# Optimization experiments

Hardware: AMD Instinct MI355X
Metric: run time of the kernel (lower is better)

Reference implementation:

```python
import jax, jax.numpy as jnp
import numpy as np

N_EMBD = 1024
N_HEAD = 16
HEAD_DIM = N_EMBD // N_HEAD
B, T = 4, 1024
EPS = 1e-5


def _linear_params(key, fan_in, fan_out):
    kw, kb = jax.random.split(key)
    bound = 1.0 / np.sqrt(fan_in)
    W = jax.random.uniform(kw, (fan_in, fan_out), minval=-bound, maxval=bound, dtype=jnp.float32)
    b = jax.random.uniform(kb, (fan_out,), minval=-bound, maxval=bound, dtype=jnp.float32)
    return W, b


def setup_inputs() -> dict:
    key = jax.random.key(0)
    ks = jax.random.split(key, 8)
    x = jax.random.normal(ks[0], (B, T, N_EMBD), dtype=jnp.float32)
    Wq, bq = _linear_params(ks[1], N_EMBD, N_EMBD)
    Wk, bk = _linear_params(ks[2], N_EMBD, N_EMBD)
    Wv, bv = _linear_params(ks[3], N_EMBD, N_EMBD)
    Wp, bp = _linear_params(ks[4], N_EMBD, N_EMBD)
    W1, b1 = _linear_params(ks[5], N_EMBD, 4 * N_EMBD)
    W2, b2 = _linear_params(ks[6], 4 * N_EMBD, N_EMBD)
    g1 = jnp.ones((N_EMBD,), jnp.float32); be1 = jnp.zeros((N_EMBD,), jnp.float32)
    g2 = jnp.ones((N_EMBD,), jnp.float32); be2 = jnp.zeros((N_EMBD,), jnp.float32)
    return {"x": x, "Wq": Wq, "bq": bq, "Wk": Wk, "bk": bk, "Wv": Wv, "bv": bv,
            "Wp": Wp, "bp": bp, "W1": W1, "b1": b1, "W2": W2, "b2": b2,
            "g1": g1, "be1": be1, "g2": g2, "be2": be2}


def _layernorm(x, g, b):
    mu = jnp.mean(x, axis=-1, keepdims=True)
    var = jnp.mean(jnp.square(x - mu), axis=-1, keepdims=True)
    return (x - mu) * jax.lax.rsqrt(var + EPS) * g + b


def _attention(x, Wq, bq, Wk, bk, Wv, bv, Wp, bp):
    Bsz, Tt, C = x.shape
    def heads(W, b):
        return (x @ W + b).reshape(Bsz, Tt, N_HEAD, HEAD_DIM).transpose(0, 2, 1, 3)  # [B,H,T,d]
    q, k, v = heads(Wq, bq), heads(Wk, bk), heads(Wv, bv)
    scores = jnp.einsum('bhqd,bhkd->bhqk', q, k) / np.sqrt(HEAD_DIM).astype(np.float32)
    causal = jnp.tril(jnp.ones((Tt, Tt), dtype=bool))
    scores = jnp.where(causal, scores, -jnp.inf)
    attn = jax.nn.softmax(scores, axis=-1)
    out = jnp.einsum('bhqk,bhkd->bhqd', attn, v)  # [B,H,T,d]
    out = out.transpose(0, 2, 1, 3).reshape(Bsz, Tt, C)
    return out @ Wp + bp


def _ff(x, W1, b1, W2, b2):
    h = jax.nn.gelu(x @ W1 + b1, approximate=False)  # torch nn.GELU default = exact erf
    return h @ W2 + b2


def reference(x, Wq, bq, Wk, bk, Wv, bv, Wp, bp, W1, b1, W2, b2, g1, be1, g2, be2):
    x = x + _attention(_layernorm(x, g1, be1), Wq, bq, Wk, bk, Wv, bv, Wp, bp)
    x = x + _ff(_layernorm(x, g2, be2), W1, b1, W2, b2)
    return x
```

## Files before the change

### kernel.cpp

```cpp
#include <hip/hip_runtime.h>
#include <hip/hip_bf16.h>

typedef __attribute__((ext_vector_type(8))) __bf16 bf16x8;
typedef __attribute__((ext_vector_type(4))) float f32x4;
typedef __attribute__((ext_vector_type(4))) unsigned short u16x4;
typedef unsigned short u16;

#define AS3(p) ((__attribute__((address_space(3))) void*)(p))
#define AS1(p) ((const __attribute__((address_space(1))) void*)(p))

__device__ __forceinline__ u16 f2b(float f) {
    __hip_bfloat16 h = __float2bfloat16(f);
    return __builtin_bit_cast(u16, h);
}

__device__ __forceinline__ float gelu_exact(float v) {
    const float z = v * 0.70710678118654752f;
    const float a = fabsf(z);
    const float t = __builtin_amdgcn_rcpf(1.0f + 0.3275911f * a);
    float p = 1.061405429f;
    p = p * t - 1.453152027f;
    p = p * t + 1.421413741f;
    p = p * t - 0.284496736f;
    p = p * t + 0.254829592f;
    p = p * t;
    float erfv = 1.0f - p * __expf(-a * a);
    erfv = copysignf(erfv, z);
    return 0.5f * v * (1.0f + erfv);
}

__global__ __launch_bounds__(256) void transpose_w(
    const float* __restrict__ W, u16* __restrict__ WT, int K, int N)
{
    __shared__ u16 tile[32][33];
    const int tx = threadIdx.x & 31, ty = threadIdx.x >> 5;
    const int n0 = blockIdx.x * 32, k0 = blockIdx.y * 32;
    #pragma unroll
    for (int p = 0; p < 4; ++p)
        tile[ty + p * 8][tx] = f2b(W[(size_t)(k0 + ty + p * 8) * N + n0 + tx]);
    __syncthreads();
    #pragma unroll
    for (int p = 0; p < 4; ++p)
        WT[(size_t)(n0 + ty + p * 8) * K + k0 + tx] = tile[tx][ty + p * 8];
}

__global__ __launch_bounds__(256) void transpose_w3(
    const float* __restrict__ W0, const float* __restrict__ W1,
    const float* __restrict__ W2, u16* __restrict__ WT)
{
    __shared__ u16 tile[32][33];
    const int z = blockIdx.z;
    const float* W = (z == 0) ? W0 : (z == 1) ? W1 : W2;
    u16* dst = WT + (size_t)z * 1024 * 1024;
    const int tx = threadIdx.x & 31, ty = threadIdx.x >> 5;
    const int n0 = blockIdx.x * 32, k0 = blockIdx.y * 32;
    #pragma unroll
    for (int p = 0; p < 4; ++p)
        tile[ty + p * 8][tx] = f2b(W[(size_t)(k0 + ty + p * 8) * 1024 + n0 + tx]);
    __syncthreads();
    #pragma unroll
    for (int p = 0; p < 4; ++p)
        dst[(size_t)(n0 + ty + p * 8) * 1024 + k0 + tx] = tile[tx][ty + p * 8];
}

__global__ __launch_bounds__(256) void ln_bf16(
    const float* __restrict__ xin, const float* __restrict__ gam,
    const float* __restrict__ bet, u16* __restrict__ yout)
{
    __shared__ float red[8];
    const int row = blockIdx.x, tid = threadIdx.x;
    float4 v = ((const float4*)(xin + (size_t)row * 1024))[tid];
    float s = v.x + v.y + v.z + v.w;
    #pragma unroll
    for (int o = 32; o > 0; o >>= 1) s += __shfl_xor(s, o, 64);
    if ((tid & 63) == 0) red[tid >> 6] = s;
    __syncthreads();
    const float mu = (red[0] + red[1] + red[2] + red[3]) * (1.f / 1024.f);
    const float dx = v.x - mu, dy = v.y - mu, dz = v.z - mu, dw = v.w - mu;
    float sq = dx * dx + dy * dy + dz * dz + dw * dw;
    #pragma unroll
    for (int o = 32; o > 0; o >>= 1) sq += __shfl_xor(sq, o, 64);
    if ((tid & 63) == 0) red[4 + (tid >> 6)] = sq;
    __syncthreads();
    const float var = (red[4] + red[5] + red[6] + red[7]) * (1.f / 1024.f);
    const float inv = rsqrtf(var + 1e-5f);
    const float4 G = ((const float4*)gam)[tid];
    const float4 Bt = ((const float4*)bet)[tid];
    u16x4 o;
    o[0] = f2b(dx * inv * G.x + Bt.x);
    o[1] = f2b(dy * inv * G.y + Bt.y);
    o[2] = f2b(dz * inv * G.z + Bt.z);
    o[3] = f2b(dw * inv * G.w + Bt.w);
    ((u16x4*)(yout + (size_t)row * 1024))[tid] = o;
}

template <int MODE, int BM>
__global__ __launch_bounds__(256, (BM == 128 ? 3 : 2)) void gemm_bf16(
    const u16* __restrict__ A, const u16* __restrict__ BT,
    const float* __restrict__ b0, const float* __restrict__ b1,
    const float* __restrict__ b2, const float* __restrict__ resid,
    void* __restrict__ outp, int M, int N, int K)
{
    constexpr int WM = BM / 2;
    constexpr int MI = WM / 16;
    constexpr int NI = 4;
    constexpr int AJ = BM / 64;
    constexpr int AELEM = BM * 32;
    constexpr int BELEM = 128 * 32;
    __shared__ u16 Asm[3 * AELEM];
    __shared__ u16 Bsm[3 * BELEM];

    const int tid = threadIdx.x;
    const int lane = tid & 63, wid = tid >> 6;
    const int wm = wid >> 1, wn = wid & 1;
    const int g = lane >> 4, l16 = lane & 15;
    const int sx = (l16 >> 1) & 3;
    const int sslot = (lane & 3) ^ ((lane >> 3) & 3);

    const int nBN = N >> 7;
    const int cpx = gridDim.x >> 3;
    const int wg = (blockIdx.x & 7) * cpx + (blockIdx.x >> 3);
    const int bm0 = (wg / nBN) * BM, bn0 = (wg % nBN) * 128;

    f32x4 acc[MI][NI] = {};

    const u16* aBase = A + (size_t)(bm0 + (lane >> 2)) * K + sslot * 8;
    const u16* bBase = BT + (size_t)(bn0 + (lane >> 2)) * K + sslot * 8;

    auto stage = [&](int kt, int buf) {
        u16* adst = Asm + buf * AELEM + lane * 8;
        u16* bdst = Bsm + buf * BELEM + lane * 8;
        #pragma unroll
        for (int j = 0; j < AJ; ++j) {
            const int ia = wid * AJ + j;
            __builtin_amdgcn_global_load_lds(AS1(aBase + (size_t)(ia * 16) * K + kt),
                                             AS3(adst + ia * 512), 16, 0, 0);
        }
        #pragma unroll
        for (int j = 0; j < 2; ++j) {
            const int ib = wid * 2 + j;
            __builtin_amdgcn_global_load_lds(AS1(bBase + (size_t)(ib * 16) * K + kt),
                                             AS3(bdst + ib * 512), 16, 0, 0);
        }
    };

    const int nt = K / 32;
    stage(0, 0);
    stage(32, 1);
    int cur = 0, pre = 2;

    for (int t = 0; t < nt; ++t) {
        if (t + 1 < nt) {
            if constexpr (BM == 256) asm volatile("s_waitcnt vmcnt(6)" ::: "memory");
            else                     asm volatile("s_waitcnt vmcnt(4)" ::: "memory");
        } else {
            asm volatile("s_waitcnt vmcnt(0)" ::: "memory");
        }
        __builtin_amdgcn_s_barrier();
        __builtin_amdgcn_sched_barrier(0);

        const u16* asrc = Asm + cur * AELEM;
        const u16* bsrc = Bsm + cur * BELEM;
        bf16x8 af[MI], bfr[NI];
        #pragma unroll
        for (int mi = 0; mi < MI; ++mi) {
            const int r = wm * WM + mi * 16 + l16;
            af[mi] = *(const bf16x8*)(asrc + r * 32 + ((g ^ sx) << 3));
        }
        #pragma unroll
        for (int ni = 0; ni < NI; ++ni) {
            const int c = wn * 64 + ni * 16 + l16;
            bfr[ni] = *(const bf16x8*)(bsrc + c * 32 + ((g ^ sx) << 3));
        }
        if (t + 2 < nt) stage((t + 2) * 32, pre);

        #pragma unroll
        for (int mi = 0; mi < MI; ++mi)
            #pragma unroll
            for (int ni = 0; ni < NI; ++ni)
                acc[mi][ni] = __builtin_amdgcn_mfma_f32_16x16x32_bf16(
                    af[mi], bfr[ni], acc[mi][ni], 0, 0, 0);

        pre = cur;
        cur = (cur == 2) ? 0 : cur + 1;
    }

    #pragma unroll
    for (int mi = 0; mi < MI; ++mi) {
        #pragma unroll
        for (int ni = 0; ni < NI; ++ni) {
            #pragma unroll
            for (int j = 0; j < 4; ++j) {
                const int m = bm0 + wm * WM + mi * 16 + g * 4 + j;
                const int n = bn0 + wn * 64 + ni * 16 + l16;
                float v = acc[mi][ni][j];
                if constexpr (MODE == 0) {
                    const float bias = (n < 1024) ? b0[n]
                                      : (n < 2048) ? b1[n - 1024] : b2[n - 2048];
                    ((u16*)outp)[(size_t)m * N + n] = f2b(v + bias);
                } else if constexpr (MODE == 1) {
                    ((float*)outp)[(size_t)m * N + n] =
                        v + b0[n] + resid[(size_t)m * N + n];
                } else {
                    ((u16*)outp)[(size_t)m * N + n] = f2b(gelu_exact(v + b0[n]));
                }
            }
        }
    }
}

__global__ __launch_bounds__(256) void attn_fwd(
    const u16* __restrict__ qkv, u16* __restrict__ outp)
{
    __shared__ u16 Ksm[64 * 72];
    __shared__ u16 Vsm[64 * 72];
    __shared__ u16 Psm[4][16 * 72];
    const int tid = threadIdx.x, lane = tid & 63, w = tid >> 6;
    const int lin = blockIdx.y * 8 + blockIdx.x;
    const int xq = (lin >> 3) & 7;
    const int bh = (((lin >> 6) & 7) << 3) | (lin & 7);
    const int b = bh >> 4, h = bh & 15;
    const int g = lane >> 4, l16 = lane & 15;
    const int skv = tid >> 4;
    const int sd4 = (tid & 15) * 4;

    const u16* kvb = qkv + (size_t)(b * 1024) * 3072 + 1024 + h * 64;

    u16x4 kreg[4], vreg[4];
    auto issue = [&](int kv0) {
        const u16* kb = kvb + (size_t)kv0 * 3072;
        #pragma unroll
        for (int i = 0; i < 4; ++i)
            kreg[i] = *(const u16x4*)(kb + (size_t)(skv + 16 * i) * 3072 + sd4);
        #pragma unroll
        for (int i = 0; i < 4; ++i)
            vreg[i] = *(const u16x4*)(kb + (size_t)(4 * skv + i) * 3072 + 1024 + sd4);
    };

    #pragma unroll
    for (int half = 0; half < 2; ++half) {
        const int qt = half ? (15 - xq) : xq;
        const int q0 = qt * 64;

        bf16x8 qf0, qf1;
        {
            const u16* qp = qkv + (size_t)(b * 1024 + q0 + w * 16 + l16) * 3072
                            + h * 64 + g * 8;
            qf0 = *(const bf16x8*)qp;
            qf1 = *(const bf16x8*)(qp + 32);
        }
        float m_run[4] = {-1e30f, -1e30f, -1e30f, -1e30f};
        float l_run[4] = {0.f, 0.f, 0.f, 0.f};
        f32x4 oacc[4] = {};

        issue(0);

        for (int kvt = 0; kvt <= qt; ++kvt) {
            const int kv0 = kvt * 64;
            __syncthreads();
            #pragma unroll
            for (int i = 0; i < 4; ++i)
                *(u16x4*)(Ksm + (skv + 16 * i) * 72 + sd4) = kreg[i];
            #pragma unroll
            for (int j = 0; j < 4; ++j) {
                u16x4 t;
                t[0] = vreg[0][j]; t[1] = vreg[1][j];
                t[2] = vreg[2][j]; t[3] = vreg[3][j];
                *(u16x4*)(Vsm + (sd4 + j) * 72 + 4 * skv) = t;
            }
            __syncthreads();
            if (kvt < qt) issue(kv0 + 64);

            f32x4 s[4];
            #pragma unroll
            for (int t = 0; t < 4; ++t) {
                const bf16x8 kf0 = *(const bf16x8*)(Ksm + (t * 16 + l16) * 72 + g * 8);
                const bf16x8 kf1 = *(const bf16x8*)(Ksm + (t * 16 + l16) * 72 + 32 + g * 8);
                f32x4 z = {};
                z = __builtin_amdgcn_mfma_f32_16x16x32_bf16(qf0, kf0, z, 0, 0, 0);
                z = __builtin_amdgcn_mfma_f32_16x16x32_bf16(qf1, kf1, z, 0, 0, 0);
                s[t] = z;
            }
            float mx[4] = {-1e30f, -1e30f, -1e30f, -1e30f};
            #pragma unroll
            for (int t = 0; t < 4; ++t)
                #pragma unroll
                for (int j = 0; j < 4; ++j) {
                    const int qrow = q0 + w * 16 + g * 4 + j;
                    const int kvc = kv0 + t * 16 + l16;
                    float v = s[t][j] * 0.125f;
                    if (kvc > qrow) v = -1e30f;
                    s[t][j] = v;
                    mx[j] = fmaxf(mx[j], v);
                }
            #pragma unroll
            for (int o = 1; o < 16; o <<= 1)
                #pragma unroll
                for (int j = 0; j < 4; ++j)
                    mx[j] = fmaxf(mx[j], __shfl_xor(mx[j], o, 16));
            float alpha[4], rs[4];
            #pragma unroll
            for (int j = 0; j < 4; ++j) {
                const float mn = fmaxf(m_run[j], mx[j]);
                alpha[j] = __expf(m_run[j] - mn);
                m_run[j] = mn;
                rs[j] = 0.f;
            }
            #pragma unroll
            for (int t = 0; t < 4; ++t)
                #pragma unroll
                for (int j = 0; j < 4; ++j) {
                    const float p = __expf(s[t][j] - m_run[j]);
                    s[t][j] = p;
                    rs[j] += p;
                }
            #pragma unroll
            for (int o = 1; o < 16; o <<= 1)
                #pragma unroll
                for (int j = 0; j < 4; ++j)
                    rs[j] += __shfl_xor(rs[j], o, 16);
            #pragma unroll
            for (int j = 0; j < 4; ++j)
                l_run[j] = l_run[j] * alpha[j] + rs[j];
            #pragma unroll
            for (int dt = 0; dt < 4; ++dt)
                #pragma unroll
                for (int j = 0; j < 4; ++j)
                    oacc[dt][j] *= alpha[j];
            #pragma unroll
            for (int t = 0; t < 4; ++t)
                #pragma unroll
                for (int j = 0; j < 4; ++j)
                    Psm[w][(g * 4 + j) * 72 + t * 16 + l16] = f2b(s[t][j]);
            const bf16x8 pf0 = *(const bf16x8*)(&Psm[w][l16 * 72 + g * 8]);
            const bf16x8 pf1 = *(const bf16x8*)(&Psm[w][l16 * 72 + 32 + g * 8]);
            #pragma unroll
            for (int dt = 0; dt < 4; ++dt) {
                const bf16x8 vf0 = *(const bf16x8*)(Vsm + (dt * 16 + l16) * 72 + g * 8);
                const bf16x8 vf1 = *(const bf16x8*)(Vsm + (dt * 16 + l16) * 72 + 32 + g * 8);
                oacc[dt] = __builtin_amdgcn_mfma_f32_16x16x32_bf16(pf0, vf0, oacc[dt], 0, 0, 0);
                oacc[dt] = __builtin_amdgcn_mfma_f32_16x16x32_bf16(pf1, vf1, oacc[dt], 0, 0, 0);
            }
        }
        #pragma unroll
        for (int dt = 0; dt < 4; ++dt)
            #pragma unroll
            for (int j = 0; j < 4; ++j) {
                const int m = b * 1024 + q0 + w * 16 + g * 4 + j;
                const int col = h * 64 + dt * 16 + l16;
                outp[(size_t)m * 1024 + col] = f2b(oacc[dt][j] / l_run[j]);
            }
    }
}

extern "C" void kernel_launch(void* const* d_in, const int* in_sizes, int n_in,
                              void* d_out, int out_size, void* d_ws, size_t ws_size,
                              hipStream_t stream)
{
    const float* x   = (const float*)d_in[0];
    const float* Wq  = (const float*)d_in[1];
    const float* bq  = (const float*)d_in[2];
    const float* Wk  = (const float*)d_in[3];
    const float* bk  = (const float*)d_in[4];
    const float* Wv  = (const float*)d_in[5];
    const float* bv  = (const float*)d_in[6];
    const float* Wp  = (const float*)d_in[7];
    const float* bp  = (const float*)d_in[8];
    const float* W1  = (const float*)d_in[9];
    const float* b1  = (const float*)d_in[10];
    const float* W2  = (const float*)d_in[11];
    const float* b2  = (const float*)d_in[12];
    const float* g1  = (const float*)d_in[13];
    const float* be1 = (const float*)d_in[14];
    const float* g2  = (const float*)d_in[15];
    const float* be2 = (const float*)d_in[16];

    char* ws = (char*)d_ws;
    const size_t MB = 1024 * 1024;
    u16*   ln_buf = (u16*)(ws);
    u16*   qkv    = (u16*)(ws + 8 * MB);
    u16*   attn_o = (u16*)(ws + 32 * MB);
    float* x1     = (float*)(ws + 40 * MB);
    u16*   hbuf   = (u16*)(ws + 56 * MB);
    u16*   wqkvT  = (u16*)(ws + 88 * MB);
    u16*   wpT    = (u16*)(ws + 94 * MB);
    u16*   w1T    = (u16*)(ws + 96 * MB);
    u16*   w2T    = (u16*)(ws + 104 * MB);

    transpose_w3<<<dim3(32, 32, 3), 256, 0, stream>>>(Wq, Wk, Wv, wqkvT);
    transpose_w<<<dim3(32, 32), 256, 0, stream>>>(Wp, wpT, 1024, 1024);
    transpose_w<<<dim3(128, 32), 256, 0, stream>>>(W1, w1T, 1024, 4096);
    transpose_w<<<dim3(32, 128), 256, 0, stream>>>(W2, w2T, 4096, 1024);

    ln_bf16<<<4096, 256, 0, stream>>>(x, g1, be1, ln_buf);
    gemm_bf16<0, 256><<<384, 256, 0, stream>>>(
        ln_buf, wqkvT, bq, bk, bv, nullptr, qkv, 4096, 3072, 1024);
    attn_fwd<<<dim3(8, 64), 256, 0, stream>>>(qkv, attn_o);
    gemm_bf16<1, 128><<<256, 256, 0, stream>>>(
        attn_o, wpT, bp, nullptr, nullptr, x, x1, 4096, 1024, 1024);
    ln_bf16<<<4096, 256, 0, stream>>>(x1, g2, be2, ln_buf);
    gemm_bf16<2, 256><<<512, 256, 0, stream>>>(
        ln_buf, w1T, b1, nullptr, nullptr, nullptr, hbuf, 4096, 4096, 1024);
    gemm_bf16<1, 128><<<256, 256, 0, stream>>>(
        hbuf, w2T, b2, nullptr, nullptr, x1, (float*)d_out, 4096, 1024, 4096);
}
```

Baseline: 228.2 us.

## Split-K the N=1024 GEMMs and fuse partial reduction with residual and LayerNorm

The two N=1024 GEMMs (attention projection and FF2) now use split-K by 2, writing fp32 partial sums that a new reduce_ln kernel (proj + bias + residual + LayerNorm2) or reduce_add kernel (FF2 + bias + residual) combines. This doubles the workgroup count for those GEMMs, which previously launched only 256 blocks, to fill more CUs. The separate LayerNorm2 launch is folded into the reduction. The QKV GEMM also switches from BM=256 to BM=128 with 768 blocks. The cost is extra fp32 partial-sum traffic to and from global memory, plus one more kernel launch for the final residual add.

```diff
diff --git a/kernel.cpp b/kernel.cpp
--- a/kernel.cpp
+++ b/kernel.cpp
@@ -94,11 +94,66 @@
     ((u16x4*)(yout + (size_t)row * 1024))[tid] = o;
 }
 
-template <int MODE, int BM>
+__global__ __launch_bounds__(256) void reduce_ln(
+    const float* __restrict__ p0, const float* __restrict__ p1,
+    const float* __restrict__ bias, const float* __restrict__ resid,
+    const float* __restrict__ gam, const float* __restrict__ bet,
+    float* __restrict__ xout, u16* __restrict__ yout)
+{
+    __shared__ float red[8];
+    const int row = blockIdx.x, tid = threadIdx.x;
+    const size_t off = (size_t)row * 256 + tid;
+    float4 a = ((const float4*)p0)[off];
+    const float4 b = ((const float4*)p1)[off];
+    const float4 r = ((const float4*)resid)[off];
+    const float4 bs = ((const float4*)bias)[tid];
+    a.x += b.x + r.x + bs.x; a.y += b.y + r.y + bs.y;
+    a.z += b.z + r.z + bs.z; a.w += b.w + r.w + bs.w;
+    ((float4*)xout)[off] = a;
+    float s = a.x + a.y + a.z + a.w;
+    #pragma unroll
+    for (int o = 32; o > 0; o >>= 1) s += __shfl_xor(s, o, 64);
+    if ((tid & 63) == 0) red[tid >> 6] = s;
+    __syncthreads();
+    const float mu = (red[0] + red[1] + red[2] + red[3]) * (1.f / 1024.f);
+    const float dx = a.x - mu, dy = a.y - mu, dz = a.z - mu, dw = a.w - mu;
+    float sq = dx * dx + dy * dy + dz * dz + dw * dw;
+    #pragma unroll
+    for (int o = 32; o > 0; o >>= 1) sq += __shfl_xor(sq, o, 64);
+    if ((tid & 63) == 0) red[4 + (tid >> 6)] = sq;
+    __syncthreads();
+    const float var = (red[4] + red[5] + red[6] + red[7]) * (1.f / 1024.f);
+    const float inv = rsqrtf(var + 1e-5f);
+    const float4 G = ((const float4*)gam)[tid];
+    const float4 Bt = ((const float4*)bet)[tid];
+    u16x4 o;
+    o[0] = f2b(dx * inv * G.x + Bt.x);
+    o[1] = f2b(dy * inv * G.y + Bt.y);
+    o[2] = f2b(dz * inv * G.z + Bt.z);
+    o[3] = f2b(dw * inv * G.w + Bt.w);
+    ((u16x4*)(yout + (size_t)row * 1024))[tid] = o;
+}
+
+__global__ __launch_bounds__(256) void reduce_add(
+    const float* __restrict__ p0, const float* __restrict__ p1,
+    const float* __restrict__ bias, const float* __restrict__ resid,
+    float* __restrict__ out)
+{
+    const size_t i = (size_t)blockIdx.x * 256 + threadIdx.x;
+    float4 a = ((const float4*)p0)[i];
+    const float4 b = ((const float4*)p1)[i];
+    const float4 r = ((const float4*)resid)[i];
+    const float4 bs = ((const float4*)bias)[i & 255];
+    a.x += b.x + r.x + bs.x; a.y += b.y + r.y + bs.y;
+    a.z += b.z + r.z + bs.z; a.w += b.w + r.w + bs.w;
+    ((float4*)out)[i] = a;
+}
+
+template <int MODE, int BM, int SK>
 __global__ __launch_bounds__(256, (BM == 128 ? 3 : 2)) void gemm_bf16(
     const u16* __restrict__ A, const u16* __restrict__ BT,
     const float* __restrict__ b0, const float* __restrict__ b1,
-    const float* __restrict__ b2, const float* __restrict__ resid,
+    const float* __restrict__ b2,
     void* __restrict__ outp, int M, int N, int K)
 {
     constexpr int WM = BM / 2;
@@ -118,14 +173,18 @@
     const int sslot = (lane & 3) ^ ((lane >> 3) & 3);
 
     const int nBN = N >> 7;
+    const int per = (M / BM) * nBN;
     const int cpx = gridDim.x >> 3;
     const int wg = (blockIdx.x & 7) * cpx + (blockIdx.x >> 3);
-    const int bm0 = (wg / nBN) * BM, bn0 = (wg % nBN) * 128;
+    const int skid = (SK > 1) ? (wg / per) : 0;
+    const int rem = wg - skid * per;
+    const int bm0 = (rem / nBN) * BM, bn0 = (rem % nBN) * 128;
+    const int kb = skid * (K / SK);
 
     f32x4 acc[MI][NI] = {};
 
-    const u16* aBase = A + (size_t)(bm0 + (lane >> 2)) * K + sslot * 8;
-    const u16* bBase = BT + (size_t)(bn0 + (lane >> 2)) * K + sslot * 8;
+    const u16* aBase = A + (size_t)(bm0 + (lane >> 2)) * K + kb + sslot * 8;
+    const u16* bBase = BT + (size_t)(bn0 + (lane >> 2)) * K + kb + sslot * 8;
 
     auto stage = [&](int kt, int buf) {
         u16* adst = Asm + buf * AELEM + lane * 8;
@@ -144,7 +203,7 @@
         }
     };
 
-    const int nt = K / 32;
+    const int nt = K / (32 * SK);
     stage(0, 0);
     stage(32, 1);
     int cur = 0, pre = 2;
@@ -198,11 +257,11 @@
                     const float bias = (n < 1024) ? b0[n]
                                       : (n < 2048) ? b1[n - 1024] : b2[n - 2048];
                     ((u16*)outp)[(size_t)m * N + n] = f2b(v + bias);
-                } else if constexpr (MODE == 1) {
-                    ((float*)outp)[(size_t)m * N + n] =
-                        v + b0[n] + resid[(size_t)m * N + n];
+                } else if constexpr (MODE == 2) {
+                    ((u16*)outp)[(size_t)m * N + n] = f2b(gelu_exact(v + b0[n]));
                 } else {
-                    ((u16*)outp)[(size_t)m * N + n] = f2b(gelu_exact(v + b0[n]));
+                    float* pout = (float*)outp + (size_t)skid * M * N;
+                    pout[(size_t)m * N + n] = v;
                 }
             }
         }
@@ -386,6 +445,8 @@
     u16*   wpT    = (u16*)(ws + 94 * MB);
     u16*   w1T    = (u16*)(ws + 96 * MB);
     u16*   w2T    = (u16*)(ws + 104 * MB);
+    float* projP  = (float*)(ws + 56 * MB);
+    float* ff2P   = (float*)(ws + 8 * MB);
 
     transpose_w3<<<dim3(32, 32, 3), 256, 0, stream>>>(Wq, Wk, Wv, wqkvT);
     transpose_w<<<dim3(32, 32), 256, 0, stream>>>(Wp, wpT, 1024, 1024);
@@ -393,14 +454,17 @@
     transpose_w<<<dim3(32, 128), 256, 0, stream>>>(W2, w2T, 4096, 1024);
 
     ln_bf16<<<4096, 256, 0, stream>>>(x, g1, be1, ln_buf);
-    gemm_bf16<0, 256><<<384, 256, 0, stream>>>(
-        ln_buf, wqkvT, bq, bk, bv, nullptr, qkv, 4096, 3072, 1024);
+    gemm_bf16<0, 128, 1><<<768, 256, 0, stream>>>(
+        ln_buf, wqkvT, bq, bk, bv, qkv, 4096, 3072, 1024);
     attn_fwd<<<dim3(8, 64), 256, 0, stream>>>(qkv, attn_o);
-    gemm_bf16<1, 128><<<256, 256, 0, stream>>>(
-        attn_o, wpT, bp, nullptr, nullptr, x, x1, 4096, 1024, 1024);
-    ln_bf16<<<4096, 256, 0, stream>>>(x1, g2, be2, ln_buf);
-    gemm_bf16<2, 256><<<512, 256, 0, stream>>>(
-        ln_buf, w1T, b1, nullptr, nullptr, nullptr, hbuf, 4096, 4096, 1024);
-    gemm_bf16<1, 128><<<256, 256, 0, stream>>>(
-        hbuf, w2T, b2, nullptr, nullptr, x1, (float*)d_out, 4096, 1024, 4096);
-}
+    gemm_bf16<3, 128, 2><<<512, 256, 0, stream>>>(
+        attn_o, wpT, nullptr, nullptr, nullptr, projP, 4096, 1024, 1024);
+    reduce_ln<<<4096, 256, 0, stream>>>(
+        projP, projP + 4096 * 1024, bp, x, g2, be2, x1, ln_buf);
+    gemm_bf16<2, 256, 1><<<512, 256, 0, stream>>>(
+        ln_buf, w1T, b1, nullptr, nullptr, hbuf, 4096, 4096, 1024);
+    gemm_bf16<3, 128, 2><<<512, 256, 0, stream>>>(
+        hbuf, w2T, nullptr, nullptr, nullptr, ff2P, 4096, 1024, 4096);
+    reduce_add<<<4096, 256, 0, stream>>>(
+        ff2P, ff2P + 4096 * 1024, b2, x1, (float*)d_out);
+}
```

Measured after the change: 221.4 us. -3.0%, faster.
